# Optimization experiments

Hardware: AMD Instinct MI355X
Metric: run time of the kernel (lower is better)

The kernel has to match this reference:

```python
import jax, jax.numpy as jnp
import numpy as np

N_HEAD = 16

def setup_inputs() -> dict:
    key = jax.random.key(0)
    ks = jax.random.split(key, 5)
    B, T, D = 2, 2048, 1024
    k = D // N_HEAD
    scale = 0.02
    return {
        'x': jax.random.normal(ks[0], (B, T, D), dtype=jnp.float32),
        'Wq': jax.random.normal(ks[1], (D, D), dtype=jnp.float32) * scale,
        'Wk': jax.random.normal(ks[2], (D, k), dtype=jnp.float32) * scale,
        'Wv': jax.random.normal(ks[3], (D, k), dtype=jnp.float32) * scale,
        'Wo': jax.random.normal(ks[4], (D, D), dtype=jnp.float32) * scale,
    }

def reference(x, Wq, Wk, Wv, Wo):
    B, T, D = x.shape
    h = N_HEAD
    k = D // h
    Q = (x @ Wq).reshape(B, T, h, k)          # per-head queries
    K = x @ Wk                                 # single shared K head: (B,T,k)
    V = x @ Wv                                 # single shared V head: (B,T,k)
    scores = jnp.einsum('bthk,bsk->bhts', Q, K) / jnp.sqrt(jnp.float32(k))
    causal = jnp.tril(jnp.ones((T, T), dtype=bool))  # (T,T)
    scores = jnp.where(causal[None, None, :, :], scores, -jnp.inf)
    A = jax.nn.softmax(scores, axis=-1)        # (B,h,T,T)
    Y = jnp.einsum('bhts,bsk->bthk', A, V).reshape(B, T, D)
    return Y @ Wo
```

## Files before the change

### kernel.cpp

```cpp
#include <hip/hip_runtime.h>
#include <hip/hip_bf16.h>
#include <stdint.h>

typedef short short8 __attribute__((ext_vector_type(8)));
typedef float f32x4 __attribute__((ext_vector_type(4)));

constexpr int SEQ   = 2048;
constexpr int DM    = 1024;
constexpr int NHEAD = 16;
constexpr int HD    = 64;
constexpr int LDQ   = 1152;
constexpr int BATCH = 2;

__device__ __forceinline__ unsigned short f2bf(float f) {
    union { float f; uint32_t u; } v; v.f = f;
    uint32_t u = v.u;
    uint32_t r = (u + 0x7fffu + ((u >> 16) & 1u)) >> 16;
    return (unsigned short)r;
}

typedef __attribute__((address_space(1))) const void gvoid_t;
typedef __attribute__((address_space(3))) void lvoid_t;
__device__ __forceinline__ void gload16(const void* g, void* l) {
    __builtin_amdgcn_global_load_lds((gvoid_t*)g, (lvoid_t*)l, 16, 0, 0);
}

__global__ __launch_bounds__(256) void cast_x_kernel(
        const float* __restrict__ x, unsigned short* __restrict__ xb, int n) {
    int i = (blockIdx.x * 256 + threadIdx.x) * 4;
    if (i >= n) return;
    const float4 v = *(const float4*)(x + i);
    ushort4 o;
    o.x = f2bf(v.x); o.y = f2bf(v.y); o.z = f2bf(v.z); o.w = f2bf(v.w);
    *(ushort4*)(xb + i) = o;
}

__global__ __launch_bounds__(256) void prep_w_kernel(
        const float* __restrict__ Wq, const float* __restrict__ Wk,
        const float* __restrict__ Wv, const float* __restrict__ Wo,
        unsigned short* __restrict__ wtq, unsigned short* __restrict__ wot) {
    __shared__ unsigned short tile[32][33];
    int z = blockIdx.z;
    const float* W; unsigned short* Wt; int C;
    if (z == 0)      { W = Wq; Wt = wtq;                              C = DM; }
    else if (z == 1) { W = Wk; Wt = wtq + (size_t)DM * DM;            C = HD; }
    else if (z == 2) { W = Wv; Wt = wtq + (size_t)(DM + HD) * DM;     C = HD; }
    else             { W = Wo; Wt = wot;                              C = DM; }
    int c0 = blockIdx.x * 32, r0 = blockIdx.y * 32;
    if (c0 >= C) return;
    int tx = threadIdx.x & 31, ty = threadIdx.x >> 5;
    for (int i = ty; i < 32; i += 8)
        tile[i][tx] = f2bf(W[(size_t)(r0 + i) * C + (c0 + tx)]);
    __syncthreads();
    for (int i = ty; i < 32; i += 8)
        Wt[(size_t)(c0 + i) * DM + (r0 + tx)] = tile[tx][i];
}

__global__ __launch_bounds__(256) void gemm_bt_kernel(
        const unsigned short* __restrict__ A,
        const unsigned short* __restrict__ Bt,
        void* __restrict__ Cout,
        unsigned short* __restrict__ VtOut,
        int M, int N, int K, int out_bf16) {
    __shared__ unsigned short ldsA[2][64 * 64];
    __shared__ unsigned short ldsB[2][64 * 64];
    int lane = threadIdx.x & 63, wave = threadIdx.x >> 6;
    int ln = lane & 15, quad = lane >> 4;
    int wm = wave >> 1, wn = wave & 1;
    int m0 = blockIdx.y * 64, n0 = blockIdx.x * 64;

    int t = threadIdx.x;
    int trow = t >> 3, tcb = t & 7;
    int gcb = tcb ^ (trow & 7);
    const unsigned short* gA = A + (size_t)(m0 + trow) * K + gcb * 8;
    const unsigned short* gA2 = gA + (size_t)32 * K;
    const unsigned short* gB = Bt + (size_t)(n0 + trow) * K + gcb * 8;
    const unsigned short* gB2 = gB + (size_t)32 * K;
    int dst = t * 8;

    auto stage = [&](int k0, int buf) {
        gload16(gA + k0, &ldsA[buf][dst]);
        gload16(gA2 + k0, &ldsA[buf][dst + 2048]);
        gload16(gB + k0, &ldsB[buf][dst]);
        gload16(gB2 + k0, &ldsB[buf][dst + 2048]);
    };

    f32x4 acc[2][2];
    for (int i = 0; i < 2; ++i)
        for (int jj = 0; jj < 2; ++jj) acc[i][jj] = f32x4{0, 0, 0, 0};

    stage(0, 0);
    int niter = K >> 6;
    for (int it = 0; it < niter; ++it) {
        __syncthreads();
        if (it + 1 < niter) stage((it + 1) << 6, (it + 1) & 1);
        const unsigned short* La = ldsA[it & 1];
        const unsigned short* Lb = ldsB[it & 1];
        short8 aF[2][2], bF[2][2];
#pragma unroll
        for (int hh = 0; hh < 2; ++hh) {
            int kc = hh * 4 + quad;
#pragma unroll
            for (int mt = 0; mt < 2; ++mt)
                aF[hh][mt] = *(const short8*)&La[(wm * 32 + mt * 16 + ln) * 64 +
                                                ((kc ^ (ln & 7)) * 8)];
#pragma unroll
            for (int nt = 0; nt < 2; ++nt)
                bF[hh][nt] = *(const short8*)&Lb[(wn * 32 + nt * 16 + ln) * 64 +
                                                ((kc ^ (ln & 7)) * 8)];
        }
#pragma unroll
        for (int hh = 0; hh < 2; ++hh)
#pragma unroll
            for (int mt = 0; mt < 2; ++mt)
#pragma unroll
                for (int nt = 0; nt < 2; ++nt)
                    acc[mt][nt] = __builtin_amdgcn_mfma_f32_16x16x32_bf16(
                        aF[hh][mt], bF[hh][nt], acc[mt][nt], 0, 0, 0);
    }

    if (out_bf16) {
        unsigned short* C = (unsigned short*)Cout;
#pragma unroll
        for (int mt = 0; mt < 2; ++mt)
            for (int nt = 0; nt < 2; ++nt)
                for (int r = 0; r < 4; ++r) {
                    int row = m0 + wm * 32 + mt * 16 + quad * 4 + r;
                    int col = n0 + wn * 32 + nt * 16 + ln;
                    C[(size_t)row * N + col] = f2bf(acc[mt][nt][r]);
                }
        if (VtOut != nullptr && n0 == DM + HD) {
#pragma unroll
            for (int mt = 0; mt < 2; ++mt)
                for (int nt = 0; nt < 2; ++nt)
                    for (int r = 0; r < 4; ++r) {
                        int row = m0 + wm * 32 + mt * 16 + quad * 4 + r;
                        int d = wn * 32 + nt * 16 + ln;
                        int bb = row >> 11, s = row & 2047;
                        VtOut[((size_t)bb * HD + d) * SEQ + s] = f2bf(acc[mt][nt][r]);
                    }
        }
    } else {
        float* C = (float*)Cout;
#pragma unroll
        for (int mt = 0; mt < 2; ++mt)
            for (int nt = 0; nt < 2; ++nt)
                for (int r = 0; r < 4; ++r) {
                    int row = m0 + wm * 32 + mt * 16 + quad * 4 + r;
                    int col = n0 + wn * 32 + nt * 16 + ln;
                    C[(size_t)row * N + col] = acc[mt][nt][r];
                }
    }
}

__global__ __launch_bounds__(256) void attn_kernel(
        const unsigned short* __restrict__ QKV,
        const unsigned short* __restrict__ Vt,
        unsigned short* __restrict__ Y) {
    __shared__ unsigned short ldsK[2][64 * 64];
    __shared__ unsigned short ldsV[2][64 * 64];
    __shared__ unsigned short pbuf[4][16 * 64];

    int lane = threadIdx.x & 63, wave = threadIdx.x >> 6;
    int ln = lane & 15, quad = lane >> 4;
    int bid = blockIdx.x;
    int jg = 31 - (bid >> 5);
    int bh = bid & 31;
    int h = bh & 15, b = bh >> 4;
    int q0 = (jg * 4 + wave) * 16;
    const size_t baseRow = (size_t)b * SEQ;
    const unsigned short* Vb = Vt + (size_t)b * HD * SEQ;

    int t = threadIdx.x;
    int trow = t >> 3, tcb = t & 7;
    int cbg = tcb ^ (trow & 7);
    const unsigned short* gK = QKV + (baseRow + trow) * LDQ + DM + cbg * 8;
    const unsigned short* gV = Vb + (size_t)trow * SEQ + cbg * 8;
    int dstoff = trow * 64 + tcb * 8;

    auto stageKV = [&](int s0n, int buf) {
#pragma unroll
        for (int rr = 0; rr < 2; ++rr) {
            gload16(gK + (size_t)(s0n + 32 * rr) * LDQ, &ldsK[buf][dstoff + rr * 2048]);
            gload16(gV + (size_t)32 * rr * SEQ + s0n,   &ldsV[buf][dstoff + rr * 2048]);
        }
    };

    short8 aQ0, aQ1;
    {
        const unsigned short* qp = QKV + (baseRow + q0 + ln) * LDQ + h * HD + quad * 8;
        aQ0 = *(const short8*)(qp);
        aQ1 = *(const short8*)(qp + 32);
    }

    float lsum[4] = {0.f, 0.f, 0.f, 0.f};
    f32x4 o[4];
    for (int nt = 0; nt < 4; ++nt) o[nt] = f32x4{0, 0, 0, 0};

    const float c_exp = 0.1803368802f;
    unsigned short* pb = &pbuf[wave][0];

    auto computeStep = [&](int s0, int buf, bool partial) {
        const unsigned short* Kb = ldsK[buf];
        const unsigned short* Vf = ldsV[buf];
#pragma unroll
        for (int c = 0; c < 4; ++c) {
            int kbase = s0 + c * 16;
            if (partial && kbase > q0 + 15) {
#pragma unroll
                for (int r = 0; r < 4; ++r) {
                    int row = quad * 4 + r;
                    pb[row * 64 + (((c * 2 + (ln >> 3)) ^ (row & 7)) * 8) + (ln & 7)] = 0;
                }
                continue;
            }
            short8 k0f = *(const short8*)&Kb[(c * 16 + ln) * 64 + ((quad ^ (ln & 7)) * 8)];
            short8 k1f = *(const short8*)&Kb[(c * 16 + ln) * 64 + (((4 + quad) ^ (ln & 7)) * 8)];
            f32x4 s = {0, 0, 0, 0};
            s = __builtin_amdgcn_mfma_f32_16x16x32_bf16(aQ0, k0f, s, 0, 0, 0);
            s = __builtin_amdgcn_mfma_f32_16x16x32_bf16(aQ1, k1f, s, 0, 0, 0);
            bool diag = partial && (kbase + 15 > q0);
#pragma unroll
            for (int r = 0; r < 4; ++r) {
                float e = __builtin_exp2f(s[r] * c_exp);
                if (diag && (kbase + ln > q0 + quad * 4 + r)) e = 0.f;
                lsum[r] += e;
                int row = quad * 4 + r;
                pb[row * 64 + (((c * 2 + (ln >> 3)) ^ (row & 7)) * 8) + (ln & 7)] =
                    (unsigned short)(__float_as_uint(e) >> 16);
            }
        }
        short8 aP0 = *(const short8*)&pb[ln * 64 + ((quad ^ (ln & 7)) * 8)];
        short8 aP1 = *(const short8*)&pb[ln * 64 + (((4 + quad) ^ (ln & 7)) * 8)];
#pragma unroll
        for (int nt = 0; nt < 4; ++nt) {
            short8 v0 = *(const short8*)&Vf[(nt * 16 + ln) * 64 + ((quad ^ (ln & 7)) * 8)];
            short8 v1 = *(const short8*)&Vf[(nt * 16 + ln) * 64 + (((4 + quad) ^ (ln & 7)) * 8)];
            o[nt] = __builtin_amdgcn_mfma_f32_16x16x32_bf16(aP0, v0, o[nt], 0, 0, 0);
            o[nt] = __builtin_amdgcn_mfma_f32_16x16x32_bf16(aP1, v1, o[nt], 0, 0, 0);
        }
    };

    stageKV(0, 0);
    for (int it = 0; it < jg; ++it) {
        __syncthreads();
        stageKV((it + 1) * 64, (it + 1) & 1);
        computeStep(it * 64, it & 1, false);
    }
    __syncthreads();
    computeStep(jg * 64, jg & 1, true);

    for (int off = 1; off < 16; off <<= 1)
#pragma unroll
        for (int r = 0; r < 4; ++r) lsum[r] += __shfl_xor(lsum[r], off);
#pragma unroll
    for (int r = 0; r < 4; ++r) {
        float inv = 1.0f / lsum[r];
        int t_idx = q0 + quad * 4 + r;
        unsigned short* yp = Y + (baseRow + t_idx) * DM + h * HD + ln;
        for (int nt = 0; nt < 4; ++nt)
            yp[nt * 16] = f2bf(o[nt][r] * inv);
    }
}

extern "C" void kernel_launch(void* const* d_in, const int* in_sizes, int n_in,
                              void* d_out, int out_size, void* d_ws, size_t ws_size,
                              hipStream_t stream) {
    const float* x  = (const float*)d_in[0];
    const float* Wq = (const float*)d_in[1];
    const float* Wk = (const float*)d_in[2];
    const float* Wv = (const float*)d_in[3];
    const float* Wo = (const float*)d_in[4];
    float* out = (float*)d_out;

    char* ws = (char*)d_ws;
    unsigned short* xb  = (unsigned short*)(ws);
    unsigned short* y   = (unsigned short*)(ws);
    unsigned short* wtq = (unsigned short*)(ws + 8388608);
    unsigned short* wot = (unsigned short*)(ws + 10747904);
    unsigned short* qkv = (unsigned short*)(ws + 12845056);
    unsigned short* Vt  = (unsigned short*)(ws + 22282240);

    const int BT = BATCH * SEQ;

    hipLaunchKernelGGL(cast_x_kernel, dim3(BT * DM / 4 / 256), dim3(256), 0, stream,
                       x, xb, BT * DM);
    hipLaunchKernelGGL(prep_w_kernel, dim3(DM / 32, DM / 32, 4), dim3(256), 0, stream,
                       Wq, Wk, Wv, Wo, wtq, wot);

    hipLaunchKernelGGL(gemm_bt_kernel, dim3(LDQ / 64, BT / 64), dim3(256), 0, stream,
                       xb, wtq, (void*)qkv, Vt, BT, LDQ, DM, 1);

    hipLaunchKernelGGL(attn_kernel, dim3(32 * 32), dim3(256), 0, stream,
                       qkv, Vt, y);

    hipLaunchKernelGGL(gemm_bt_kernel, dim3(DM / 64, BT / 64), dim3(256), 0, stream,
                       y, wot, (void*)out, nullptr, BT, DM, DM, 0);
}
```

Baseline: 168.4 us.

## Keep attention probabilities in registers via transposed MFMA and lane shuffles

Computes S^T (keys x queries) by swapping the MFMA operands, so each lane holds probabilities for a single query. Those are packed to bf16 and moved with cross-lane shuffles into the B operand of a transposed P·V MFMA, which removes the per-wave LDS P buffer and its write/read round trip. The row-sum reduction becomes two shuffles instead of four rounds per row. The output is stored as 4-element vectors. This trades LDS traffic for extra shuffle and select instructions, and the diagonal masking logic is restructured per 16-key chunk.

```diff
diff --git a/kernel.cpp b/kernel.cpp
--- a/kernel.cpp
+++ b/kernel.cpp
@@ -159,7 +159,6 @@
         unsigned short* __restrict__ Y) {
     __shared__ unsigned short ldsK[2][64 * 64];
     __shared__ unsigned short ldsV[2][64 * 64];
-    __shared__ unsigned short pbuf[4][16 * 64];
 
     int lane = threadIdx.x & 63, wave = threadIdx.x >> 6;
     int ln = lane & 15, quad = lane >> 4;
@@ -193,51 +192,65 @@
         aQ1 = *(const short8*)(qp + 32);
     }
 
-    float lsum[4] = {0.f, 0.f, 0.f, 0.f};
+    float lsum = 0.f;
     f32x4 o[4];
     for (int nt = 0; nt < 4; ++nt) o[nt] = f32x4{0, 0, 0, 0};
 
     const float c_exp = 0.1803368802f;
-    unsigned short* pb = &pbuf[wave][0];
+    const int myq = q0 + ln;
+    const int srcl = (quad & 1) * 32 + ln;
+    const bool hi_cs = (quad >= 2);
 
     auto computeStep = [&](int s0, int buf, bool partial) {
         const unsigned short* Kb = ldsK[buf];
         const unsigned short* Vf = ldsV[buf];
 #pragma unroll
-        for (int c = 0; c < 4; ++c) {
-            int kbase = s0 + c * 16;
-            if (partial && kbase > q0 + 15) {
+        for (int w2 = 0; w2 < 2; ++w2) {
+            if (partial && (w2 * 32 > wave * 16 + 15)) continue;
+            unsigned pk[2][2];
+#pragma unroll
+            for (int cs = 0; cs < 2; ++cs) {
+                int c = w2 * 2 + cs;
+                if (partial && c > wave) { pk[cs][0] = 0; pk[cs][1] = 0; continue; }
+                int kbase = s0 + c * 16;
+                short8 kf0 = *(const short8*)&Kb[(c * 16 + ln) * 64 + ((quad ^ (ln & 7)) * 8)];
+                short8 kf1 = *(const short8*)&Kb[(c * 16 + ln) * 64 + (((4 + quad) ^ (ln & 7)) * 8)];
+                f32x4 s = {0, 0, 0, 0};
+                s = __builtin_amdgcn_mfma_f32_16x16x32_bf16(kf0, aQ0, s, 0, 0, 0);
+                s = __builtin_amdgcn_mfma_f32_16x16x32_bf16(kf1, aQ1, s, 0, 0, 0);
+                bool diag = partial && (c == wave);
+                float p[4];
 #pragma unroll
                 for (int r = 0; r < 4; ++r) {
-                    int row = quad * 4 + r;
-                    pb[row * 64 + (((c * 2 + (ln >> 3)) ^ (row & 7)) * 8) + (ln & 7)] = 0;
+                    float e = __builtin_exp2f(s[r] * c_exp);
+                    if (diag && (kbase + quad * 4 + r > myq)) e = 0.f;
+                    p[r] = e;
+                    lsum += e;
                 }
-                continue;
+                pk[cs][0] = (__float_as_uint(p[0]) >> 16) |
+                            (__float_as_uint(p[1]) & 0xffff0000u);
+                pk[cs][1] = (__float_as_uint(p[2]) >> 16) |
+                            (__float_as_uint(p[3]) & 0xffff0000u);
             }
-            short8 k0f = *(const short8*)&Kb[(c * 16 + ln) * 64 + ((quad ^ (ln & 7)) * 8)];
-            short8 k1f = *(const short8*)&Kb[(c * 16 + ln) * 64 + (((4 + quad) ^ (ln & 7)) * 8)];
-            f32x4 s = {0, 0, 0, 0};
-            s = __builtin_amdgcn_mfma_f32_16x16x32_bf16(aQ0, k0f, s, 0, 0, 0);
-            s = __builtin_amdgcn_mfma_f32_16x16x32_bf16(aQ1, k1f, s, 0, 0, 0);
-            bool diag = partial && (kbase + 15 > q0);
-#pragma unroll
-            for (int r = 0; r < 4; ++r) {
-                float e = __builtin_exp2f(s[r] * c_exp);
-                if (diag && (kbase + ln > q0 + quad * 4 + r)) e = 0.f;
-                lsum[r] += e;
-                int row = quad * 4 + r;
-                pb[row * 64 + (((c * 2 + (ln >> 3)) ^ (row & 7)) * 8) + (ln & 7)] =
-                    (unsigned short)(__float_as_uint(e) >> 16);
+            unsigned a00 = (unsigned)__shfl((int)pk[0][0], srcl);
+            unsigned a10 = (unsigned)__shfl((int)pk[1][0], srcl);
+            unsigned a01 = (unsigned)__shfl((int)pk[0][1], srcl);
+            unsigned a11 = (unsigned)__shfl((int)pk[1][1], srcl);
+            unsigned b00 = (unsigned)__shfl((int)pk[0][0], srcl + 16);
+            unsigned b10 = (unsigned)__shfl((int)pk[1][0], srcl + 16);
+            unsigned b01 = (unsigned)__shfl((int)pk[0][1], srcl + 16);
+            unsigned b11 = (unsigned)__shfl((int)pk[1][1], srcl + 16);
+            union { unsigned u[4]; short8 v; } bP;
+            bP.u[0] = hi_cs ? a10 : a00;
+            bP.u[1] = hi_cs ? a11 : a01;
+            bP.u[2] = hi_cs ? b10 : b00;
+            bP.u[3] = hi_cs ? b11 : b01;
+#pragma unroll
+            for (int nt = 0; nt < 4; ++nt) {
+                short8 vA = *(const short8*)&Vf[(nt * 16 + ln) * 64 +
+                                               (((w2 * 4 + quad) ^ (ln & 7)) * 8)];
+                o[nt] = __builtin_amdgcn_mfma_f32_16x16x32_bf16(vA, bP.v, o[nt], 0, 0, 0);
             }
-        }
-        short8 aP0 = *(const short8*)&pb[ln * 64 + ((quad ^ (ln & 7)) * 8)];
-        short8 aP1 = *(const short8*)&pb[ln * 64 + (((4 + quad) ^ (ln & 7)) * 8)];
-#pragma unroll
-        for (int nt = 0; nt < 4; ++nt) {
-            short8 v0 = *(const short8*)&Vf[(nt * 16 + ln) * 64 + ((quad ^ (ln & 7)) * 8)];
-            short8 v1 = *(const short8*)&Vf[(nt * 16 + ln) * 64 + (((4 + quad) ^ (ln & 7)) * 8)];
-            o[nt] = __builtin_amdgcn_mfma_f32_16x16x32_bf16(aP0, v0, o[nt], 0, 0, 0);
-            o[nt] = __builtin_amdgcn_mfma_f32_16x16x32_bf16(aP1, v1, o[nt], 0, 0, 0);
         }
     };
 
@@ -250,16 +263,18 @@
     __syncthreads();
     computeStep(jg * 64, jg & 1, true);
 
-    for (int off = 1; off < 16; off <<= 1)
-#pragma unroll
-        for (int r = 0; r < 4; ++r) lsum[r] += __shfl_xor(lsum[r], off);
-#pragma unroll
-    for (int r = 0; r < 4; ++r) {
-        float inv = 1.0f / lsum[r];
-        int t_idx = q0 + quad * 4 + r;
-        unsigned short* yp = Y + (baseRow + t_idx) * DM + h * HD + ln;
-        for (int nt = 0; nt < 4; ++nt)
-            yp[nt * 16] = f2bf(o[nt][r] * inv);
+    lsum += __shfl_xor(lsum, 16);
+    lsum += __shfl_xor(lsum, 32);
+    float inv = 1.0f / lsum;
+    unsigned short* yp = Y + (baseRow + q0 + ln) * DM + h * HD + quad * 4;
+#pragma unroll
+    for (int nt = 0; nt < 4; ++nt) {
+        ushort4 w;
+        w.x = f2bf(o[nt][0] * inv);
+        w.y = f2bf(o[nt][1] * inv);
+        w.z = f2bf(o[nt][2] * inv);
+        w.w = f2bf(o[nt][3] * inv);
+        *(ushort4*)(yp + nt * 16) = w;
     }
 }
 
```

Result: slower. 173.4 us (+3.0%).

## Remap attention blocks so waves share K/V tiles across heads

Applied to the files above, without the earlier changes.

Each block now covers a 32-row query tile for four heads (one per wave) instead of 64 query rows of one head. Because this is multi-query attention with a single shared K/V head, every staged K/V tile is reused by four heads and two 16-row query subtiles per wave, which halves the number of blocks and the K/V staging traffic. In exchange each wave holds twice the accumulators and Q fragments, raising register pressure, and the grid shrinks to 512 blocks, which may hurt occupancy or load balance on the causal tail.

```diff
diff --git a/kernel.cpp b/kernel.cpp
--- a/kernel.cpp
+++ b/kernel.cpp
@@ -164,10 +164,11 @@
     int lane = threadIdx.x & 63, wave = threadIdx.x >> 6;
     int ln = lane & 15, quad = lane >> 4;
     int bid = blockIdx.x;
-    int jg = 31 - (bid >> 5);
-    int bh = bid & 31;
-    int h = bh & 15, b = bh >> 4;
-    int q0 = (jg * 4 + wave) * 16;
+    int j = 63 - (bid >> 3);
+    int sub = bid & 7;
+    int hg = sub >> 1, b = sub & 1;
+    int h = hg * 4 + wave;
+    int q0 = j * 32;
     const size_t baseRow = (size_t)b * SEQ;
     const unsigned short* Vb = Vt + (size_t)b * HD * SEQ;
 
@@ -186,80 +187,133 @@
         }
     };
 
-    short8 aQ0, aQ1;
-    {
-        const unsigned short* qp = QKV + (baseRow + q0 + ln) * LDQ + h * HD + quad * 8;
-        aQ0 = *(const short8*)(qp);
-        aQ1 = *(const short8*)(qp + 32);
-    }
-
-    float lsum[4] = {0.f, 0.f, 0.f, 0.f};
-    f32x4 o[4];
-    for (int nt = 0; nt < 4; ++nt) o[nt] = f32x4{0, 0, 0, 0};
+    short8 aQ[2][2];
+#pragma unroll
+    for (int qi = 0; qi < 2; ++qi) {
+        const unsigned short* qp = QKV + (baseRow + q0 + qi * 16 + ln) * LDQ + h * HD + quad * 8;
+        aQ[qi][0] = *(const short8*)(qp);
+        aQ[qi][1] = *(const short8*)(qp + 32);
+    }
+
+    float lsum[2][4];
+    f32x4 o[2][4];
+#pragma unroll
+    for (int qi = 0; qi < 2; ++qi) {
+        for (int r = 0; r < 4; ++r) lsum[qi][r] = 0.f;
+        for (int nt = 0; nt < 4; ++nt) o[qi][nt] = f32x4{0, 0, 0, 0};
+    }
 
     const float c_exp = 0.1803368802f;
     unsigned short* pb = &pbuf[wave][0];
+    const int nsteps = (32 * j + 95) >> 6;
 
     auto computeStep = [&](int s0, int buf, bool partial) {
         const unsigned short* Kb = ldsK[buf];
         const unsigned short* Vf = ldsV[buf];
+        float p1[4][4];
 #pragma unroll
         for (int c = 0; c < 4; ++c) {
             int kbase = s0 + c * 16;
-            if (partial && kbase > q0 + 15) {
+            bool e0 = partial && (kbase > q0 + 15);
+            bool e1 = partial && (kbase > q0 + 31);
+            short8 kf0 = {}, kf1 = {};
+            if (!e1) {
+                kf0 = *(const short8*)&Kb[(c * 16 + ln) * 64 + ((quad ^ (ln & 7)) * 8)];
+                kf1 = *(const short8*)&Kb[(c * 16 + ln) * 64 + (((4 + quad) ^ (ln & 7)) * 8)];
+            }
+            if (e0) {
 #pragma unroll
                 for (int r = 0; r < 4; ++r) {
                     int row = quad * 4 + r;
                     pb[row * 64 + (((c * 2 + (ln >> 3)) ^ (row & 7)) * 8) + (ln & 7)] = 0;
                 }
-                continue;
-            }
-            short8 k0f = *(const short8*)&Kb[(c * 16 + ln) * 64 + ((quad ^ (ln & 7)) * 8)];
-            short8 k1f = *(const short8*)&Kb[(c * 16 + ln) * 64 + (((4 + quad) ^ (ln & 7)) * 8)];
-            f32x4 s = {0, 0, 0, 0};
-            s = __builtin_amdgcn_mfma_f32_16x16x32_bf16(aQ0, k0f, s, 0, 0, 0);
-            s = __builtin_amdgcn_mfma_f32_16x16x32_bf16(aQ1, k1f, s, 0, 0, 0);
-            bool diag = partial && (kbase + 15 > q0);
-#pragma unroll
+            } else {
+                f32x4 s = {0, 0, 0, 0};
+                s = __builtin_amdgcn_mfma_f32_16x16x32_bf16(aQ[0][0], kf0, s, 0, 0, 0);
+                s = __builtin_amdgcn_mfma_f32_16x16x32_bf16(aQ[0][1], kf1, s, 0, 0, 0);
+                bool diag = partial && (kbase + 15 > q0);
+#pragma unroll
+                for (int r = 0; r < 4; ++r) {
+                    float e = __builtin_exp2f(s[r] * c_exp);
+                    if (diag && (kbase + ln > q0 + quad * 4 + r)) e = 0.f;
+                    lsum[0][r] += e;
+                    int row = quad * 4 + r;
+                    pb[row * 64 + (((c * 2 + (ln >> 3)) ^ (row & 7)) * 8) + (ln & 7)] =
+                        (unsigned short)(__float_as_uint(e) >> 16);
+                }
+            }
+            if (e1) {
+#pragma unroll
+                for (int r = 0; r < 4; ++r) p1[c][r] = 0.f;
+            } else {
+                f32x4 s = {0, 0, 0, 0};
+                s = __builtin_amdgcn_mfma_f32_16x16x32_bf16(aQ[1][0], kf0, s, 0, 0, 0);
+                s = __builtin_amdgcn_mfma_f32_16x16x32_bf16(aQ[1][1], kf1, s, 0, 0, 0);
+                bool diag = partial && (kbase + 15 > q0 + 16);
+#pragma unroll
+                for (int r = 0; r < 4; ++r) {
+                    float e = __builtin_exp2f(s[r] * c_exp);
+                    if (diag && (kbase + ln > q0 + 16 + quad * 4 + r)) e = 0.f;
+                    lsum[1][r] += e;
+                    p1[c][r] = e;
+                }
+            }
+        }
+        short8 vr[4][2];
+#pragma unroll
+        for (int nt = 0; nt < 4; ++nt) {
+            vr[nt][0] = *(const short8*)&Vf[(nt * 16 + ln) * 64 + ((quad ^ (ln & 7)) * 8)];
+            vr[nt][1] = *(const short8*)&Vf[(nt * 16 + ln) * 64 + (((4 + quad) ^ (ln & 7)) * 8)];
+        }
+        {
+            short8 aP0 = *(const short8*)&pb[ln * 64 + ((quad ^ (ln & 7)) * 8)];
+            short8 aP1 = *(const short8*)&pb[ln * 64 + (((4 + quad) ^ (ln & 7)) * 8)];
+#pragma unroll
+            for (int nt = 0; nt < 4; ++nt) {
+                o[0][nt] = __builtin_amdgcn_mfma_f32_16x16x32_bf16(aP0, vr[nt][0], o[0][nt], 0, 0, 0);
+                o[0][nt] = __builtin_amdgcn_mfma_f32_16x16x32_bf16(aP1, vr[nt][1], o[0][nt], 0, 0, 0);
+            }
+        }
+#pragma unroll
+        for (int c = 0; c < 4; ++c)
             for (int r = 0; r < 4; ++r) {
-                float e = __builtin_exp2f(s[r] * c_exp);
-                if (diag && (kbase + ln > q0 + quad * 4 + r)) e = 0.f;
-                lsum[r] += e;
                 int row = quad * 4 + r;
                 pb[row * 64 + (((c * 2 + (ln >> 3)) ^ (row & 7)) * 8) + (ln & 7)] =
-                    (unsigned short)(__float_as_uint(e) >> 16);
-            }
-        }
-        short8 aP0 = *(const short8*)&pb[ln * 64 + ((quad ^ (ln & 7)) * 8)];
-        short8 aP1 = *(const short8*)&pb[ln * 64 + (((4 + quad) ^ (ln & 7)) * 8)];
-#pragma unroll
-        for (int nt = 0; nt < 4; ++nt) {
-            short8 v0 = *(const short8*)&Vf[(nt * 16 + ln) * 64 + ((quad ^ (ln & 7)) * 8)];
-            short8 v1 = *(const short8*)&Vf[(nt * 16 + ln) * 64 + (((4 + quad) ^ (ln & 7)) * 8)];
-            o[nt] = __builtin_amdgcn_mfma_f32_16x16x32_bf16(aP0, v0, o[nt], 0, 0, 0);
-            o[nt] = __builtin_amdgcn_mfma_f32_16x16x32_bf16(aP1, v1, o[nt], 0, 0, 0);
+                    (unsigned short)(__float_as_uint(p1[c][r]) >> 16);
+            }
+        {
+            short8 aP0 = *(const short8*)&pb[ln * 64 + ((quad ^ (ln & 7)) * 8)];
+            short8 aP1 = *(const short8*)&pb[ln * 64 + (((4 + quad) ^ (ln & 7)) * 8)];
+#pragma unroll
+            for (int nt = 0; nt < 4; ++nt) {
+                o[1][nt] = __builtin_amdgcn_mfma_f32_16x16x32_bf16(aP0, vr[nt][0], o[1][nt], 0, 0, 0);
+                o[1][nt] = __builtin_amdgcn_mfma_f32_16x16x32_bf16(aP1, vr[nt][1], o[1][nt], 0, 0, 0);
+            }
         }
     };
 
     stageKV(0, 0);
-    for (int it = 0; it < jg; ++it) {
+    for (int it = 0; it < nsteps - 1; ++it) {
         __syncthreads();
         stageKV((it + 1) * 64, (it + 1) & 1);
         computeStep(it * 64, it & 1, false);
     }
     __syncthreads();
-    computeStep(jg * 64, jg & 1, true);
-
-    for (int off = 1; off < 16; off <<= 1)
-#pragma unroll
-        for (int r = 0; r < 4; ++r) lsum[r] += __shfl_xor(lsum[r], off);
-#pragma unroll
-    for (int r = 0; r < 4; ++r) {
-        float inv = 1.0f / lsum[r];
-        int t_idx = q0 + quad * 4 + r;
-        unsigned short* yp = Y + (baseRow + t_idx) * DM + h * HD + ln;
-        for (int nt = 0; nt < 4; ++nt)
-            yp[nt * 16] = f2bf(o[nt][r] * inv);
+    computeStep((nsteps - 1) * 64, (nsteps - 1) & 1, true);
+
+#pragma unroll
+    for (int qi = 0; qi < 2; ++qi) {
+        for (int off = 1; off < 16; off <<= 1)
+#pragma unroll
+            for (int r = 0; r < 4; ++r) lsum[qi][r] += __shfl_xor(lsum[qi][r], off);
+#pragma unroll
+        for (int r = 0; r < 4; ++r) {
+            float inv = 1.0f / lsum[qi][r];
+            int t_idx = q0 + qi * 16 + quad * 4 + r;
+            unsigned short* yp = Y + (baseRow + t_idx) * DM + h * HD + ln;
+            for (int nt = 0; nt < 4; ++nt)
+                yp[nt * 16] = f2bf(o[qi][nt][r] * inv);
+        }
     }
 }
 
@@ -291,7 +345,7 @@
     hipLaunchKernelGGL(gemm_bt_kernel, dim3(LDQ / 64, BT / 64), dim3(256), 0, stream,
                        xb, wtq, (void*)qkv, Vt, BT, LDQ, DM, 1);
 
-    hipLaunchKernelGGL(attn_kernel, dim3(32 * 32), dim3(256), 0, stream,
+    hipLaunchKernelGGL(attn_kernel, dim3(512), dim3(256), 0, stream,
                        qkv, Vt, y);
 
     hipLaunchKernelGGL(gemm_bt_kernel, dim3(DM / 64, BT / 64), dim3(256), 0, stream,
```

Result: slower. 187.1 us (+11.1%).
